# Kernel optimization log

Measured on AMD Instinct MI355X. Metric: run time of the kernel, lower is better.

## Reference

```python
import jax, jax.numpy as jnp
import numpy as np

N = 50000
E = 1280000
D = 64          # in_features = hidden_size = out_features
HEADS = 1
NEG_SLOPE = 0.2
EPS_COS = 1e-8
EPS_SM = 1e-16


def _xavier(key, shape):
    fan_in, fan_out = shape[0], shape[-1]
    lim = float(np.sqrt(6.0 / (fan_in + fan_out)))
    return jax.random.uniform(key, shape, jnp.float32, -lim, lim)


def setup_inputs() -> dict:
    key = jax.random.key(0)
    ks = jax.random.split(key, 16)
    x = jax.random.normal(ks[0], (N, D), jnp.float32)
    edge_index = jax.random.randint(ks[1], (2, E), 0, N, jnp.int64)
    edge_attr = jax.random.uniform(ks[2], (E,), jnp.float32)
    return {
        "x": x,
        "edge_index": edge_index,
        "edge_attr": edge_attr,
        # COSGAT layer 0 (in D -> out D, heads=1)
        "W0": _xavier(ks[3], (D, HEADS * D)),
        "att0": _xavier(ks[4], (HEADS, 2 * D)),
        "beta0": jnp.zeros((HEADS,), jnp.float32),
        "b0": jnp.zeros((HEADS * D,), jnp.float32),
        # COSGAT layer 1
        "W1": _xavier(ks[5], (D, HEADS * D)),
        "att1": _xavier(ks[6], (HEADS, 2 * D)),
        "beta1": jnp.zeros((HEADS,), jnp.float32),
        "b1": jnp.zeros((HEADS * D,), jnp.float32),
        # LinearEncoder residual branch
        "rW1": _xavier(ks[7], (D, D)),
        "rb1": jnp.zeros((D,), jnp.float32),
        "rW2": _xavier(ks[8], (D, D)),
        "rb2": jnp.zeros((D,), jnp.float32),
    }


def _seg_softmax(logits, idx, n):
    # softmax over edges grouped by target node idx; logits [E, H]
    m = jax.ops.segment_max(logits, idx, num_segments=n)
    ex = jnp.exp(logits - m[idx])
    s = jax.ops.segment_sum(ex, idx, num_segments=n)
    return ex / (s[idx] + EPS_SM)


def _cosgat(x, src, dst, w, W, att, beta, bias):
    n = x.shape[0]
    H = (x @ W).reshape(n, HEADS, -1)           # [N, H, C]
    Hi, Hj = H[dst], H[src]                      # [E, H, C]
    # GAT logits: att . [Hi || Hj]
    logits = (jnp.einsum('ehc,hc->eh', Hi, att[:, :H.shape[-1]])
              + jnp.einsum('ehc,hc->eh', Hj, att[:, H.shape[-1]:]))
    logits = jnp.where(logits >= 0, logits, NEG_SLOPE * logits)
    # cosine similarity on original features
    xi, xj = x[dst], x[src]
    ni = jnp.maximum(jnp.linalg.norm(xi, axis=-1), EPS_COS)
    nj = jnp.maximum(jnp.linalg.norm(xj, axis=-1), EPS_COS)
    cos = jnp.sum(xi * xj, axis=-1) / (ni * nj)  # [E]
    cos = jnp.broadcast_to(cos[:, None], logits.shape)
    gat_alpha = _seg_softmax(logits, dst, n)
    cos_alpha = _seg_softmax(cos, dst, n)
    b = jax.nn.sigmoid(beta)[None, :]            # [1, H]
    fused = (1.0 - b) * gat_alpha + b * cos_alpha
    w_cl = jnp.minimum(w, 4.0)
    gate = jnp.clip(1.0 - w_cl / 4.0, 0.0, 1.0)[:, None]  # [E, 1]
    final = _seg_softmax(fused * gate, dst, n)   # [E, H]
    msg = Hj * final[:, :, None]                 # [E, H, C]
    out = jax.ops.segment_sum(msg, dst, num_segments=n)
    out = out.reshape(n, -1) + bias              # concat heads + bias
    return jax.nn.elu(out)


def reference(x, edge_index, edge_attr, W0, att0, beta0, b0,
              W1, att1, beta1, b1, rW1, rb1, rW2, rb2):
    src, dst = edge_index[0], edge_index[1]      # PyG: i = target = edge_index[1]
    # residual MLP: Linear -> relu -> Linear (dropout p=0, eval)
    x_res = jax.nn.relu(x @ rW1 + rb1) @ rW2 + rb2
    h = _cosgat(x, src, dst, edge_attr, W0, att0, beta0, b0)
    h = jax.nn.elu(h)                            # inter-layer elu in encoder
    h = _cosgat(h, src, dst, edge_attr, W1, att1, beta1, b1)
    return h + x_res
```

## Files before the change

kernel.cpp:

```cpp
#include <hip/hip_runtime.h>
#include <hip/hip_bf16.h>
#include <math.h>


constexpr int D = 64;
constexpr int CAP = 64;
constexpr float NEG_SLOPE = 0.2f;
constexpr float EPS_COS = 1e-8f;
constexpr float EPS_SM = 1e-16f;

#if defined(__has_builtin)
#if __has_builtin(__builtin_amdgcn_cvt_pk_f32_fp8) && __has_builtin(__builtin_amdgcn_cvt_pk_fp8_f32)
#define HW_FP8 1
#endif
#endif

typedef float floatx2 __attribute__((ext_vector_type(2)));

__device__ __forceinline__ float wred_sum(float v) {
#pragma unroll
  for (int off = 32; off > 0; off >>= 1) v += __shfl_xor(v, off, 64);
  return v;
}
__device__ __forceinline__ float wred_max(float v) {
#pragma unroll
  for (int off = 32; off > 0; off >>= 1) v = fmaxf(v, __shfl_xor(v, off, 64));
  return v;
}
__device__ __forceinline__ float elu1(float x) { return x > 0.f ? x : __expf(x) - 1.f; }
__device__ __forceinline__ float sane(float v) {
  return (v == v && fabsf(v) < 1e30f) ? v : 0.f;
}
__device__ __forceinline__ float ldv(const void* p, size_t i, int f32) {
  return f32 ? ((const float*)p)[i]
             : __bfloat162float(((const __hip_bfloat16*)p)[i]);
}
__device__ __forceinline__ void stv(void* p, size_t i, int f32, float v) {
  if (f32) ((float*)p)[i] = v;
  else ((__hip_bfloat16*)p)[i] = __float2bfloat16(v);
}
__device__ __forceinline__ float b2f(unsigned short u) {
  return __uint_as_float(((unsigned int)u) << 16);
}
__device__ __forceinline__ void unp8(uint4 u, float* f) {
  f[0] = __uint_as_float(u.x << 16);
  f[1] = __uint_as_float(u.x & 0xffff0000u);
  f[2] = __uint_as_float(u.y << 16);
  f[3] = __uint_as_float(u.y & 0xffff0000u);
  f[4] = __uint_as_float(u.z << 16);
  f[5] = __uint_as_float(u.z & 0xffff0000u);
  f[6] = __uint_as_float(u.w << 16);
  f[7] = __uint_as_float(u.w & 0xffff0000u);
}

__device__ __forceinline__ unsigned char enc_fp8(float v) {
#ifdef HW_FP8
  int pk = __builtin_amdgcn_cvt_pk_fp8_f32(v, v, 0, false);
  return (unsigned char)(pk & 0xFF);
#else
  _Float16 h = (_Float16)v;
  unsigned short ub;
  __builtin_memcpy(&ub, &h, 2);
  return (unsigned char)((ub + 0x80) >> 8);
#endif
}
__device__ __forceinline__ void dec_fp8x8(uint2 u, float* f) {
#ifdef HW_FP8
  floatx2 a = __builtin_amdgcn_cvt_pk_f32_fp8(u.x, false);
  floatx2 b = __builtin_amdgcn_cvt_pk_f32_fp8(u.x, true);
  floatx2 c = __builtin_amdgcn_cvt_pk_f32_fp8(u.y, false);
  floatx2 d = __builtin_amdgcn_cvt_pk_f32_fp8(u.y, true);
  f[0] = a[0]; f[1] = a[1]; f[2] = b[0]; f[3] = b[1];
  f[4] = c[0]; f[5] = c[1]; f[6] = d[0]; f[7] = d[1];
#else
#pragma unroll
  for (int i = 0; i < 8; ++i) {
    unsigned int byte = (i < 4 ? (u.x >> (8 * i)) : (u.y >> (8 * (i - 4)))) & 0xFF;
    unsigned short hb = (unsigned short)(byte << 8);
    _Float16 h;
    __builtin_memcpy(&h, &hb, 2);
    f[i] = (float)h;
  }
#endif
}

__device__ __forceinline__ unsigned int pack_sg(int src, float g) {
  int gq = (int)(g * 16383.f + 0.5f);
  return ((unsigned int)src & 0x3FFFFu) | ((unsigned int)gq << 18);
}
__device__ __forceinline__ int upk_src(unsigned int e, int N) {
  return min((int)(e & 0x3FFFFu), N - 1);
}
__device__ __forceinline__ float upk_gate(unsigned int e) {
  return (float)(e >> 18) * (1.f / 16383.f);
}
__device__ __forceinline__ float gate_of(float w) {
  return fminf(fmaxf(1.f - 0.25f * fminf(w, 4.f), 0.f), 1.f);
}

__device__ float slow_cos(const unsigned char* __restrict__ fhat, int a, int b) {
  const uint2* fa = (const uint2*)(fhat + (size_t)a * D);
  const uint2* fb = (const uint2*)(fhat + (size_t)b * D);
  float dsum = 0.f;
  for (int q = 0; q < 8; ++q) {
    float va[8], vb[8];
    dec_fp8x8(fa[q], va);
    dec_fp8x8(fb[q], vb);
#pragma unroll
    for (int i = 0; i < 8; ++i) dsum += va[i] * vb[i];
  }
  return dsum;
}

__device__ __forceinline__ void prep_node(float f, int f32, int wid, int lane,
                                          const void* __restrict__ W,
                                          const void* __restrict__ att,
                                          unsigned char* __restrict__ fhat,
                                          __hip_bfloat16* __restrict__ Hmat,
                                          float* __restrict__ a_l,
                                          float* __restrict__ a_r,
                                          float* __restrict__ ls) {
  float n2 = wred_sum(f * f);
  float nrm = fmaxf(sqrtf(n2), EPS_COS);
  fhat[(size_t)wid * D + lane] = enc_fp8(f / nrm);
  ls[lane] = f;
  __syncthreads();
  float h0 = 0.f, h1 = 0.f, h2 = 0.f, h3 = 0.f;
  if (f32) {
    const float* Wf = (const float*)W;
#pragma unroll 4
    for (int k = 0; k < D; k += 4) {
      h0 += ls[k] * Wf[k * D + lane];
      h1 += ls[k + 1] * Wf[(k + 1) * D + lane];
      h2 += ls[k + 2] * Wf[(k + 2) * D + lane];
      h3 += ls[k + 3] * Wf[(k + 3) * D + lane];
    }
  } else {
    const __hip_bfloat16* Wb = (const __hip_bfloat16*)W;
#pragma unroll 4
    for (int k = 0; k < D; k += 4) {
      h0 += ls[k] * __bfloat162float(Wb[k * D + lane]);
      h1 += ls[k + 1] * __bfloat162float(Wb[(k + 1) * D + lane]);
      h2 += ls[k + 2] * __bfloat162float(Wb[(k + 2) * D + lane]);
      h3 += ls[k + 3] * __bfloat162float(Wb[(k + 3) * D + lane]);
    }
  }
  float Hc = (h0 + h1) + (h2 + h3);
  Hmat[(size_t)wid * D + lane] = __float2bfloat16(Hc);
  float al = wred_sum(Hc * ldv(att, lane, f32));
  float ar = wred_sum(Hc * ldv(att, D + lane, f32));
  if (lane == 0) {
    a_l[wid] = al;
    a_r[wid] = ar;
  }
  __syncthreads();
}

__global__ void __launch_bounds__(256) k_bin(const unsigned short* __restrict__ xu,
                                             const int* __restrict__ ei,
                                             const void* __restrict__ w,
                                             int* __restrict__ flags,
                                             int* __restrict__ cnt,
                                             unsigned int* __restrict__ csr2,
                                             int N, int E) {
  __shared__ int sf[2];
  const int tid = threadIdx.x;
  if (tid < 64) {
    float v = b2f(xu[tid]);
    float a = fabsf(v);
    unsigned long long m = __ballot(a > 1e-4f && a < 100.f);
    unsigned long long m2 = __ballot(ei[2 * tid + 1] != 0);
    if (tid == 0) {
      sf[0] = (__popcll(m) >= 60) ? 0 : 1;
      sf[1] = (m2 == 0ull) ? 1 : 0;
      if (blockIdx.x == 0) {
        flags[0] = sf[0];
        flags[1] = sf[1];
      }
    }
  }
  __syncthreads();
  const int f32 = sf[0], wide = sf[1];
  const int e0 = (blockIdx.x * 256 + tid) * 2;
  if (e0 >= E) return;
  const bool has1 = (e0 + 1 < E);
  int s0, s1, d0, d1;
  if (wide) {
    int4 vs = *(const int4*)(ei + 2 * (size_t)e0);
    int4 vd = *(const int4*)(ei + 2 * (size_t)E + 2 * (size_t)e0);
    s0 = vs.x; s1 = vs.z; d0 = vd.x; d1 = vd.z;
  } else {
    int2 vs = *(const int2*)(ei + e0);
    int2 vd = *(const int2*)(ei + (size_t)E + e0);
    s0 = vs.x; s1 = vs.y; d0 = vd.x; d1 = vd.y;
  }
  float w0, w1 = 0.f;
  if (f32) {
    float2 wv = *(const float2*)((const float*)w + e0);
    w0 = wv.x; w1 = wv.y;
  } else {
    const __hip_bfloat16* wb = (const __hip_bfloat16*)w;
    w0 = __bfloat162float(wb[e0]);
    if (has1) w1 = __bfloat162float(wb[e0 + 1]);
  }
  int d0c = min(max(d0, 0), N - 1);
  int slot0 = atomicAdd(&cnt[d0c], 1);
  if (slot0 < CAP)
    csr2[(size_t)d0c * CAP + slot0] = pack_sg(min(max(s0, 0), N - 1), gate_of(w0));
  if (has1) {
    int d1c = min(max(d1, 0), N - 1);
    int slot1 = atomicAdd(&cnt[d1c], 1);
    if (slot1 < CAP)
      csr2[(size_t)d1c * CAP + slot1] = pack_sg(min(max(s1, 0), N - 1), gate_of(w1));
  }
}

__global__ void __launch_bounds__(64, 4) k_prepW(const void* __restrict__ xin,
                                                 const void* __restrict__ W,
                                                 const void* __restrict__ att,
                                                 const int* __restrict__ flags,
                                                 unsigned char* __restrict__ fhat,
                                                 __hip_bfloat16* __restrict__ Hmat,
                                                 float* __restrict__ a_l,
                                                 float* __restrict__ a_r, int N) {
  __shared__ float ls[D];
  const int lane = threadIdx.x;
  const int f32 = flags[0];
  float wreg[D];
  if (f32) {
    const float* Wf = (const float*)W;
#pragma unroll
    for (int k = 0; k < D; ++k) wreg[k] = Wf[k * D + lane];
  } else {
    const __hip_bfloat16* Wb = (const __hip_bfloat16*)W;
#pragma unroll
    for (int k = 0; k < D; ++k) wreg[k] = __bfloat162float(Wb[k * D + lane]);
  }
  const float attl = ldv(att, lane, f32);
  const float attr = ldv(att, D + lane, f32);
  float f = (blockIdx.x < (unsigned)N) ? ldv(xin, (size_t)blockIdx.x * D + lane, f32) : 0.f;
  for (int wid = blockIdx.x; wid < N; wid += gridDim.x) {
    const int nwid = wid + gridDim.x;
    float fnx = (nwid < N) ? ldv(xin, (size_t)nwid * D + lane, f32) : 0.f;
    float n2 = wred_sum(f * f);
    float nrm = fmaxf(sqrtf(n2), EPS_COS);
    fhat[(size_t)wid * D + lane] = enc_fp8(f / nrm);
    ls[lane] = f;
    __syncthreads();
    float h0 = 0.f, h1 = 0.f, h2 = 0.f, h3 = 0.f;
#pragma unroll
    for (int k = 0; k < D; k += 4) {
      h0 += ls[k] * wreg[k];
      h1 += ls[k + 1] * wreg[k + 1];
      h2 += ls[k + 2] * wreg[k + 2];
      h3 += ls[k + 3] * wreg[k + 3];
    }
    float Hc = (h0 + h1) + (h2 + h3);
    Hmat[(size_t)wid * D + lane] = __float2bfloat16(Hc);
    float al = wred_sum(Hc * attl);
    float ar = wred_sum(Hc * attr);
    if (lane == 0) {
      a_l[wid] = al;
      a_r[wid] = ar;
    }
    __syncthreads();
    f = fnx;
  }
}

__global__ void __launch_bounds__(64, 3) k_resW(const void* __restrict__ xin,
                                                const void* __restrict__ rW1,
                                                const void* __restrict__ rb1,
                                                const void* __restrict__ rW2,
                                                const void* __restrict__ rb2,
                                                const int* __restrict__ flags,
                                                float* __restrict__ xres, int N) {
  __shared__ float ls[D];
  const int lane = threadIdx.x;
  const int f32 = flags[0];
  float w1reg[D], w2reg[D];
  if (f32) {
    const float* w1 = (const float*)rW1;
    const float* w2 = (const float*)rW2;
#pragma unroll
    for (int k = 0; k < D; ++k) w1reg[k] = w1[k * D + lane];
#pragma unroll
    for (int k = 0; k < D; ++k) w2reg[k] = w2[k * D + lane];
  } else {
    const __hip_bfloat16* w1 = (const __hip_bfloat16*)rW1;
    const __hip_bfloat16* w2 = (const __hip_bfloat16*)rW2;
#pragma unroll
    for (int k = 0; k < D; ++k) w1reg[k] = __bfloat162float(w1[k * D + lane]);
#pragma unroll
    for (int k = 0; k < D; ++k) w2reg[k] = __bfloat162float(w2[k * D + lane]);
  }
  const float b1v = ldv(rb1, lane, f32);
  const float b2v = ldv(rb2, lane, f32);
  float f = (blockIdx.x < (unsigned)N) ? ldv(xin, (size_t)blockIdx.x * D + lane, f32) : 0.f;
  for (int wid = blockIdx.x; wid < N; wid += gridDim.x) {
    const int nwid = wid + gridDim.x;
    float fnx = (nwid < N) ? ldv(xin, (size_t)nwid * D + lane, f32) : 0.f;
    ls[lane] = f;
    __syncthreads();
    float h0 = b1v, h1 = 0.f, h2 = 0.f, h3 = 0.f;
#pragma unroll
    for (int k = 0; k < D; k += 4) {
      h0 += ls[k] * w1reg[k];
      h1 += ls[k + 1] * w1reg[k + 1];
      h2 += ls[k + 2] * w1reg[k + 2];
      h3 += ls[k + 3] * w1reg[k + 3];
    }
    float tr = fmaxf((h0 + h1) + (h2 + h3), 0.f);
    __syncthreads();
    ls[lane] = tr;
    __syncthreads();
    float g0 = b2v, g1 = 0.f, g2 = 0.f, g3 = 0.f;
#pragma unroll
    for (int k = 0; k < D; k += 4) {
      g0 += ls[k] * w2reg[k];
      g1 += ls[k + 1] * w2reg[k + 1];
      g2 += ls[k + 2] * w2reg[k + 2];
      g3 += ls[k + 3] * w2reg[k + 3];
    }
    xres[(size_t)wid * D + lane] = (g0 + g1) + (g2 + g3);
    __syncthreads();
    f = fnx;
  }
}

__global__ void __launch_bounds__(64) k_prep(const void* __restrict__ xin,
                                             const void* __restrict__ W,
                                             const void* __restrict__ att,
                                             const int* __restrict__ flags,
                                             unsigned char* __restrict__ fhat,
                                             __hip_bfloat16* __restrict__ Hmat,
                                             float* __restrict__ a_l,
                                             float* __restrict__ a_r, int N) {
  __shared__ float ls[D];
  const int lane = threadIdx.x;
  const int wid = blockIdx.x;
  if (wid >= N) return;
  const int f32 = flags[0];
  float f = ldv(xin, (size_t)wid * D + lane, f32);
  prep_node(f, f32, wid, lane, W, att, fhat, Hmat, a_l, a_r, ls);
}

__global__ void __launch_bounds__(64, 8) k_edge(const int* __restrict__ cnt,
                                                const unsigned int* __restrict__ csr2,
                                                const int* __restrict__ ei,
                                                const void* __restrict__ w,
                                                const unsigned char* __restrict__ fhat,
                                                const __hip_bfloat16* __restrict__ Hmat,
                                                const float* __restrict__ a_l,
                                                const float* __restrict__ a_r,
                                                const void* __restrict__ beta,
                                                const void* __restrict__ bias,
                                                const void* __restrict__ x,
                                                const void* __restrict__ rW1,
                                                const void* __restrict__ rb1,
                                                const void* __restrict__ rW2,
                                                const void* __restrict__ rb2,
                                                const void* __restrict__ Wn,
                                                const void* __restrict__ attn,
                                                unsigned char* __restrict__ fh2,
                                                __hip_bfloat16* __restrict__ Hm2,
                                                float* __restrict__ al2,
                                                float* __restrict__ ar2,
                                                const float* __restrict__ xres,
                                                const int* __restrict__ flags,
                                                void* __restrict__ out,
                                                int N, int E, int mode) {
  const int lane = threadIdx.x;
  const int wid = blockIdx.x;
  __shared__ float2 lc[CAP];
  __shared__ float2 sg[CAP];
  __shared__ float lds_t[D];
  if (wid >= N) return;
  const int f32 = flags[0];
  const int g = lane >> 3;
  const int sub = lane & 7;
  const int degRaw = cnt[wid];
  const float aln = a_l[wid];
  const float bb = 1.f / (1.f + __expf(-ldv(beta, 0, f32)));
  const float ob = 1.f - bb;
  const char* HmatB = (const char*)Hmat;

  float v;
  if (degRaw <= CAP) {
    const int deg = degRaw;
    const int s = wid * CAP;
    float fn[8];
    dec_fp8x8(*(const uint2*)(fhat + (((unsigned)wid << 6) | ((unsigned)sub << 3))), fn);

    float m1 = -1e30f, m2 = -1e30f;
    uint4 hm[4];
#pragma unroll
    for (int kk = 0; kk < 4; ++kk) {
      const int base = kk * 8;
      if (base < deg) {
        const int j = base + g;
        const bool val = j < deg;
        const unsigned int en = val ? csr2[s + j] : (unsigned int)wid;
        const unsigned src = (unsigned)upk_src(en, N);
        float hv[8];
        dec_fp8x8(*(const uint2*)(fhat + ((src << 6) | ((unsigned)sub << 3))), hv);
        hm[kk] = *(const uint4*)(HmatB + ((src << 7) | ((unsigned)sub << 4)));
        float d = 0.f;
#pragma unroll
        for (int i = 0; i < 8; ++i) d += fn[i] * hv[i];
        d += __shfl_xor(d, 1, 64);
        d += __shfl_xor(d, 2, 64);
        d += __shfl_xor(d, 4, 64);
        float l = aln + a_r[src];
        l = (l >= 0.f) ? l : NEG_SLOPE * l;
        if (val) {
          m1 = fmaxf(m1, l);
          m2 = fmaxf(m2, d);
          if (sub == 0) lc[j] = make_float2(l, d);
        }
      }
    }
    for (int base = 32; base < deg; base += 8) {
      const int j = base + g;
      const bool val = j < deg;
      const unsigned int en = val ? csr2[s + j] : (unsigned int)wid;
      const unsigned src = (unsigned)upk_src(en, N);
      float hv[8];
      dec_fp8x8(*(const uint2*)(fhat + ((src << 6) | ((unsigned)sub << 3))), hv);
      float d = 0.f;
#pragma unroll
      for (int i = 0; i < 8; ++i) d += fn[i] * hv[i];
      d += __shfl_xor(d, 1, 64);
      d += __shfl_xor(d, 2, 64);
      d += __shfl_xor(d, 4, 64);
      float l = aln + a_r[src];
      l = (l >= 0.f) ? l : NEG_SLOPE * l;
      if (val) {
        m1 = fmaxf(m1, l);
        m2 = fmaxf(m2, d);
        if (sub == 0) lc[j] = make_float2(l, d);
      }
    }
    m1 = fmaxf(m1, __shfl_xor(m1, 8, 64));
    m1 = fmaxf(m1, __shfl_xor(m1, 16, 64));
    m1 = fmaxf(m1, __shfl_xor(m1, 32, 64));
    m2 = fmaxf(m2, __shfl_xor(m2, 8, 64));
    m2 = fmaxf(m2, __shfl_xor(m2, 16, 64));
    m2 = fmaxf(m2, __shfl_xor(m2, 32, 64));

    float el0 = 0.f, ec0 = 0.f, gg0 = 0.f;
    int q0 = 0;
    float ps1 = 0.f, ps2 = 0.f;
    if (lane < deg) {
      const unsigned int en = csr2[s + lane];
      q0 = upk_src(en, N);
      gg0 = upk_gate(en);
      float2 t = lc[lane];
      el0 = __expf(t.x - m1);
      ec0 = __expf(t.y - m2);
      ps1 = el0;
      ps2 = ec0;
    }
    const float rs1 = 1.f / (wred_sum(ps1) + EPS_SM);
    const float rs2 = 1.f / (wred_sum(ps2) + EPS_SM);

    float sp = 0.f;
    if (lane < deg) {
      float tt = (ob * el0 * rs1 + bb * ec0 * rs2) * gg0;
      float p0 = __expf(tt - 1.f);
      sp = p0;
      sg[lane] = make_float2(__int_as_float(q0), p0);
    }
    const float rinv = 1.f / (wred_sum(sp) + EPS_SM);

    float acc[8] = {0.f, 0.f, 0.f, 0.f, 0.f, 0.f, 0.f, 0.f};
#pragma unroll
    for (int kk = 0; kk < 4; ++kk) {
      const int base = kk * 8;
      if (base < deg) {
        const int j = base + g;
        const float pv = (j < deg) ? sg[j].y : 0.f;
        float hv[8];
        unp8(hm[kk], hv);
#pragma unroll
        for (int i = 0; i < 8; ++i) acc[i] += pv * hv[i];
      }
    }
    for (int base = 32; base < deg; base += 8) {
      const int j = base + g;
      float2 en = (j < deg) ? sg[j] : make_float2(__int_as_float(wid), 0.f);
      const float pv = en.y;
      const unsigned srcv = (unsigned)__float_as_int(en.x);
      float hv[8];
      unp8(*(const uint4*)(HmatB + ((srcv << 7) | ((unsigned)sub << 4))), hv);
#pragma unroll
      for (int i = 0; i < 8; ++i) acc[i] += pv * hv[i];
    }
#pragma unroll
    for (int i = 0; i < 8; ++i) {
      acc[i] += __shfl_xor(acc[i], 8, 64);
      acc[i] += __shfl_xor(acc[i], 16, 64);
      acc[i] += __shfl_xor(acc[i], 32, 64);
    }
    if (g == 0) {
#pragma unroll
      for (int i = 0; i < 8; ++i) lds_t[8 * sub + i] = acc[i];
    }
    v = lds_t[lane] * rinv + ldv(bias, lane, f32);
  } else {
    const int wide = flags[1];
    lds_t[lane] = 0.f;
    float m1 = -1e30f, m2 = -1e30f;
    for (int e64 = lane; e64 < E; e64 += 64) {
      int dd = wide ? ei[2 * (size_t)E + 2 * (size_t)e64] : ei[(size_t)E + e64];
      if (dd != wid) continue;
      int ss = wide ? ei[2 * (size_t)e64] : ei[e64];
      ss = min(max(ss, 0), N - 1);
      float l = aln + a_r[ss];
      l = (l >= 0.f) ? l : NEG_SLOPE * l;
      float c = slow_cos(fhat, wid, ss);
      m1 = fmaxf(m1, l);
      m2 = fmaxf(m2, c);
    }
    m1 = wred_max(m1);
    m2 = wred_max(m2);
    float ps1 = 0.f, ps2 = 0.f;
    for (int e64 = lane; e64 < E; e64 += 64) {
      int dd = wide ? ei[2 * (size_t)E + 2 * (size_t)e64] : ei[(size_t)E + e64];
      if (dd != wid) continue;
      int ss = wide ? ei[2 * (size_t)e64] : ei[e64];
      ss = min(max(ss, 0), N - 1);
      float l = aln + a_r[ss];
      l = (l >= 0.f) ? l : NEG_SLOPE * l;
      float c = slow_cos(fhat, wid, ss);
      ps1 += __expf(l - m1);
      ps2 += __expf(c - m2);
    }
    const float rs1 = 1.f / (wred_sum(ps1) + EPS_SM);
    const float rs2 = 1.f / (wred_sum(ps2) + EPS_SM);
    float sp = 0.f;
    for (int e64 = lane; e64 < E; e64 += 64) {
      int dd = wide ? ei[2 * (size_t)E + 2 * (size_t)e64] : ei[(size_t)E + e64];
      if (dd != wid) continue;
      int ss = wide ? ei[2 * (size_t)e64] : ei[e64];
      ss = min(max(ss, 0), N - 1);
      float l = aln + a_r[ss];
      l = (l >= 0.f) ? l : NEG_SLOPE * l;
      float c = slow_cos(fhat, wid, ss);
      float gx = gate_of(ldv(w, e64, f32));
      float px = __expf((ob * __expf(l - m1) * rs1 + bb * __expf(c - m2) * rs2) * gx - 1.f);
      sp += px;
      for (int q = 0; q < D; ++q)
        atomicAdd(&lds_t[q], px * __bfloat162float(Hmat[(size_t)ss * D + q]));
    }
    const float rinv = 1.f / (wred_sum(sp) + EPS_SM);
    v = lds_t[lane] * rinv + ldv(bias, lane, f32);
  }

  v = elu1(v);
  if (mode == 3) {
    float a2 = xres[(size_t)wid * D + lane];
    stv(out, (size_t)wid * D + lane, f32, sane(v + a2));
  } else if (mode == 1) {
    float xv = ldv(x, (size_t)wid * D + lane, f32);
    float b0_ = ldv(rb1, lane, f32);
    __syncthreads();
    lds_t[lane] = xv;
    __syncthreads();
    float a2;
    float h0 = 0.f, h1 = 0.f, h2 = 0.f, h3 = 0.f;
    if (f32) {
      const float* w1 = (const float*)rW1;
      const float* w2 = (const float*)rW2;
#pragma unroll 4
      for (int k = 0; k < D; k += 4) {
        h0 += lds_t[k] * w1[k * D + lane];
        h1 += lds_t[k + 1] * w1[(k + 1) * D + lane];
        h2 += lds_t[k + 2] * w1[(k + 2) * D + lane];
        h3 += lds_t[k + 3] * w1[(k + 3) * D + lane];
      }
      float tr = fmaxf(b0_ + (h0 + h1) + (h2 + h3), 0.f);
      __syncthreads();
      lds_t[lane] = tr;
      __syncthreads();
      float g0 = 0.f, g1 = 0.f, g2 = 0.f, g3 = 0.f;
#pragma unroll 4
      for (int k = 0; k < D; k += 4) {
        g0 += lds_t[k] * w2[k * D + lane];
        g1 += lds_t[k + 1] * w2[(k + 1) * D + lane];
        g2 += lds_t[k + 2] * w2[(k + 2) * D + lane];
        g3 += lds_t[k + 3] * w2[(k + 3) * D + lane];
      }
      a2 = ((const float*)rb2)[lane] + (g0 + g1) + (g2 + g3);
    } else {
      const __hip_bfloat16* w1 = (const __hip_bfloat16*)rW1;
      const __hip_bfloat16* w2 = (const __hip_bfloat16*)rW2;
#pragma unroll 4
      for (int k = 0; k < D; k += 4) {
        h0 += lds_t[k] * __bfloat162float(w1[k * D + lane]);
        h1 += lds_t[k + 1] * __bfloat162float(w1[(k + 1) * D + lane]);
        h2 += lds_t[k + 2] * __bfloat162float(w1[(k + 2) * D + lane]);
        h3 += lds_t[k + 3] * __bfloat162float(w1[(k + 3) * D + lane]);
      }
      float tr = fmaxf(b0_ + (h0 + h1) + (h2 + h3), 0.f);
      __syncthreads();
      lds_t[lane] = tr;
      __syncthreads();
      float g0 = 0.f, g1 = 0.f, g2 = 0.f, g3 = 0.f;
#pragma unroll 4
      for (int k = 0; k < D; k += 4) {
        g0 += lds_t[k] * __bfloat162float(w2[k * D + lane]);
        g1 += lds_t[k + 1] * __bfloat162float(w2[(k + 1) * D + lane]);
        g2 += lds_t[k + 2] * __bfloat162float(w2[(k + 2) * D + lane]);
        g3 += lds_t[k + 3] * __bfloat162float(w2[(k + 3) * D + lane]);
      }
      a2 = __bfloat162float(((const __hip_bfloat16*)rb2)[lane]) + (g0 + g1) + (g2 + g3);
    }
    stv(out, (size_t)wid * D + lane, f32, sane(v + a2));
  } else {
    v = elu1(v);
    if (mode == 0) {
      __syncthreads();
      prep_node(sane(v), f32, wid, lane, Wn, attn, fh2, Hm2, al2, ar2, lds_t);
    } else {
      stv(out, (size_t)wid * D + lane, f32, sane(v));
    }
  }
}

extern "C" void kernel_launch(void* const* d_in, const int* in_sizes, int n_in,
                              void* d_out, int out_size, void* d_ws, size_t ws_size,
                              hipStream_t stream) {
  const void* x = d_in[0];
  const int* ei = (const int*)d_in[1];
  const void* w = d_in[2];
  const void* W0 = d_in[3];
  const void* att0 = d_in[4];
  const void* beta0 = d_in[5];
  const void* b0 = d_in[6];
  const void* W1 = d_in[7];
  const void* att1 = d_in[8];
  const void* beta1 = d_in[9];
  const void* b1 = d_in[10];
  const void* rW1 = d_in[11];
  const void* rb1 = d_in[12];
  const void* rW2 = d_in[13];
  const void* rb2 = d_in[14];

  const int N = in_sizes[0] / D;
  const int E = in_sizes[2];

  char* base = (char*)d_ws;
  size_t off = 0;
  auto alloc = [&](size_t bytes) -> void* {
    void* p = base + off;
    off += (bytes + 255) & ~(size_t)255;
    return p;
  };
  int* flags = (int*)alloc(256);
  int* cnt = (int*)alloc((size_t)N * 4);
  unsigned int* csr2 = (unsigned int*)alloc((size_t)N * CAP * 4);
  unsigned char* fhat = (unsigned char*)alloc((size_t)N * D);
  __hip_bfloat16* Hmat = (__hip_bfloat16*)alloc((size_t)N * D * 2);
  float* a_l = (float*)alloc((size_t)N * 4);
  float* a_r = (float*)alloc((size_t)N * 4);
  const size_t common_off = off;
  float* hbuf = (float*)alloc((size_t)N * D * 4);
  float* xres = (float*)alloc((size_t)N * D * 4);
  const bool tierA = (off <= ws_size);
  off = common_off;
  unsigned char* fhat2 = (unsigned char*)alloc((size_t)N * D);
  __hip_bfloat16* Hmat2 = (__hip_bfloat16*)alloc((size_t)N * D * 2);
  float* a_l2 = (float*)alloc((size_t)N * 4);
  float* a_r2 = (float*)alloc((size_t)N * 4);
  const bool tierB = (off <= ws_size);

  const int eb2 = (E / 2 + 255) / 256;

  hipMemsetAsync(cnt, 0, (size_t)N * 4, stream);
  k_bin<<<eb2, 256, 0, stream>>>((const unsigned short*)x, ei, w, flags, cnt,
                                 csr2, N, E);

  if (tierA) {
    k_prepW<<<4096, 64, 0, stream>>>(x, W0, att0, flags, fhat, Hmat, a_l, a_r, N);
    k_resW<<<3072, 64, 0, stream>>>(x, rW1, rb1, rW2, rb2, flags, xres, N);
    k_edge<<<N, 64, 0, stream>>>(cnt, csr2, ei, w, fhat, Hmat, a_l, a_r,
                                 beta0, b0, x, rW1, rb1, rW2, rb2,
                                 nullptr, nullptr, nullptr, nullptr, nullptr, nullptr,
                                 nullptr, flags, hbuf, N, E, 2);
    k_prepW<<<4096, 64, 0, stream>>>(hbuf, W1, att1, flags, fhat, Hmat, a_l, a_r, N);
    k_edge<<<N, 64, 0, stream>>>(cnt, csr2, ei, w, fhat, Hmat, a_l, a_r,
                                 beta1, b1, x, rW1, rb1, rW2, rb2,
                                 nullptr, nullptr, nullptr, nullptr, nullptr, nullptr,
                                 xres, flags, d_out, N, E, 3);
  } else if (tierB) {
    k_prep<<<N, 64, 0, stream>>>(x, W0, att0, flags, fhat, Hmat, a_l, a_r, N);
    k_edge<<<N, 64, 0, stream>>>(cnt, csr2, ei, w, fhat, Hmat, a_l, a_r,
                                 beta0, b0, x, rW1, rb1, rW2, rb2,
                                 W1, att1, fhat2, Hmat2, a_l2, a_r2,
                                 nullptr, flags, d_out, N, E, 0);
    k_edge<<<N, 64, 0, stream>>>(cnt, csr2, ei, w, fhat2, Hmat2, a_l2, a_r2,
                                 beta1, b1, x, rW1, rb1, rW2, rb2,
                                 nullptr, nullptr, nullptr, nullptr, nullptr, nullptr,
                                 nullptr, flags, d_out, N, E, 1);
  } else {
    k_prep<<<N, 64, 0, stream>>>(x, W0, att0, flags, fhat, Hmat, a_l, a_r, N);
    k_edge<<<N, 64, 0, stream>>>(cnt, csr2, ei, w, fhat, Hmat, a_l, a_r,
                                 beta0, b0, x, rW1, rb1, rW2, rb2,
                                 nullptr, nullptr, nullptr, nullptr, nullptr, nullptr,
                                 nullptr, flags, d_out, N, E, 2);
    k_prep<<<N, 64, 0, stream>>>(d_out, W1, att1, flags, fhat, Hmat, a_l, a_r, N);
    k_edge<<<N, 64, 0, stream>>>(cnt, csr2, ei, w, fhat, Hmat, a_l, a_r,
                                 beta1, b1, x, rW1, rb1, rW2, rb2,
                                 nullptr, nullptr, nullptr, nullptr, nullptr, nullptr,
                                 nullptr, flags, d_out, N, E, 1);
  }
}
```

Measured before the change: 366.3 us.

## Fuse edge binning, layer-0 prep and residual MLP into one kernel with bucketed scatter

Replaces the separate k_bin, k_prepW and k_resW launches with a single per-node kernel. Each block bins a slice of edges and then does node prep plus the residual MLP. Edges are first appended to coarse destination buckets and a follow-up k_bucket kernel scatters them into per-node CSR slots. This is meant to localize the atomics and CSR writes and to cut launch count. The cost is an extra bucket buffer and kernel, and the residual weights are now read from global memory per node instead of being held in registers across a persistent loop.

New measurement: 604.2 us. 1.65x slower.

```diff
diff --git a/kernel.cpp b/kernel.cpp
--- a/kernel.cpp
+++ b/kernel.cpp
@@ -5,6 +5,7 @@
 
 constexpr int D = 64;
 constexpr int CAP = 64;
+constexpr int NBK = 1024;
 constexpr float NEG_SLOPE = 0.2f;
 constexpr float EPS_COS = 1e-8f;
 constexpr float EPS_SM = 1e-16f;
@@ -154,6 +155,135 @@
     a_r[wid] = ar;
   }
   __syncthreads();
+}
+
+__global__ void __launch_bounds__(64) k_all(const unsigned short* __restrict__ xu,
+                                            const int* __restrict__ ei,
+                                            const void* __restrict__ w,
+                                            int* __restrict__ flags,
+                                            int* __restrict__ cnt,
+                                            int* __restrict__ bcnt,
+                                            uint2* __restrict__ bkt, int bcap,
+                                            const void* __restrict__ x,
+                                            const void* __restrict__ W,
+                                            const void* __restrict__ att,
+                                            const void* __restrict__ rW1,
+                                            const void* __restrict__ rb1,
+                                            const void* __restrict__ rW2,
+                                            const void* __restrict__ rb2,
+                                            unsigned char* __restrict__ fhat,
+                                            __hip_bfloat16* __restrict__ Hmat,
+                                            float* __restrict__ a_l,
+                                            float* __restrict__ a_r,
+                                            float* __restrict__ xres,
+                                            unsigned int* __restrict__ csr2,
+                                            int N, int E) {
+  __shared__ float ls[D];
+  const int lane = threadIdx.x;
+  const int b = blockIdx.x;
+  float dv = b2f(xu[lane]);
+  float da = fabsf(dv);
+  unsigned long long m = __ballot(da > 1e-4f && da < 100.f);
+  unsigned long long m2 = __ballot(ei[2 * lane + 1] != 0);
+  const int f32 = (__popcll(m) >= 60) ? 0 : 1;
+  const int wide = (m2 == 0ull) ? 1 : 0;
+  if (b == 0 && lane == 0) {
+    flags[0] = f32;
+    flags[1] = wide;
+  }
+  const long long e0 = ((long long)b * E) / N;
+  const long long e1 = ((long long)(b + 1) * E) / N;
+  for (long long e = e0 + lane; e < e1; e += 64) {
+    int ss, dd;
+    if (wide) {
+      ss = ei[2 * e];
+      dd = ei[2 * (size_t)E + 2 * e];
+    } else {
+      ss = ei[e];
+      dd = ei[(size_t)E + e];
+    }
+    float we = ldv(w, (size_t)e, f32);
+    const int dc = min(max(dd, 0), N - 1);
+    const unsigned int sg = pack_sg(min(max(ss, 0), N - 1), gate_of(we));
+    bool direct = true;
+    if (bcap > 0) {
+      const int bu = (int)(((long long)dc * NBK) / N);
+      const int pos = atomicAdd(&bcnt[bu], 1);
+      if (pos < bcap) {
+        bkt[(size_t)bu * bcap + pos] = make_uint2(sg, (unsigned)dc);
+        direct = false;
+      }
+    }
+    if (direct) {
+      const int slot = atomicAdd(&cnt[dc], 1);
+      if (slot < CAP) csr2[(size_t)dc * CAP + slot] = sg;
+    }
+  }
+  if (b >= N) return;
+  float f = ldv(x, (size_t)b * D + lane, f32);
+  prep_node(f, f32, b, lane, W, att, fhat, Hmat, a_l, a_r, ls);
+  ls[lane] = f;
+  __syncthreads();
+  float h0 = ldv(rb1, lane, f32), h1 = 0.f, h2 = 0.f, h3 = 0.f;
+  if (f32) {
+    const float* w1 = (const float*)rW1;
+#pragma unroll 4
+    for (int k = 0; k < D; k += 4) {
+      h0 += ls[k] * w1[k * D + lane];
+      h1 += ls[k + 1] * w1[(k + 1) * D + lane];
+      h2 += ls[k + 2] * w1[(k + 2) * D + lane];
+      h3 += ls[k + 3] * w1[(k + 3) * D + lane];
+    }
+  } else {
+    const __hip_bfloat16* w1 = (const __hip_bfloat16*)rW1;
+#pragma unroll 4
+    for (int k = 0; k < D; k += 4) {
+      h0 += ls[k] * __bfloat162float(w1[k * D + lane]);
+      h1 += ls[k + 1] * __bfloat162float(w1[(k + 1) * D + lane]);
+      h2 += ls[k + 2] * __bfloat162float(w1[(k + 2) * D + lane]);
+      h3 += ls[k + 3] * __bfloat162float(w1[(k + 3) * D + lane]);
+    }
+  }
+  float tr = fmaxf((h0 + h1) + (h2 + h3), 0.f);
+  __syncthreads();
+  ls[lane] = tr;
+  __syncthreads();
+  float g0 = ldv(rb2, lane, f32), g1 = 0.f, g2 = 0.f, g3 = 0.f;
+  if (f32) {
+    const float* w2 = (const float*)rW2;
+#pragma unroll 4
+    for (int k = 0; k < D; k += 4) {
+      g0 += ls[k] * w2[k * D + lane];
+      g1 += ls[k + 1] * w2[(k + 1) * D + lane];
+      g2 += ls[k + 2] * w2[(k + 2) * D + lane];
+      g3 += ls[k + 3] * w2[(k + 3) * D + lane];
+    }
+  } else {
+    const __hip_bfloat16* w2 = (const __hip_bfloat16*)rW2;
+#pragma unroll 4
+    for (int k = 0; k < D; k += 4) {
+      g0 += ls[k] * __bfloat162float(w2[k * D + lane]);
+      g1 += ls[k + 1] * __bfloat162float(w2[(k + 1) * D + lane]);
+      g2 += ls[k + 2] * __bfloat162float(w2[(k + 2) * D + lane]);
+      g3 += ls[k + 3] * __bfloat162float(w2[(k + 3) * D + lane]);
+    }
+  }
+  xres[(size_t)b * D + lane] = (g0 + g1) + (g2 + g3);
+}
+
+__global__ void __launch_bounds__(256) k_bucket(const int* __restrict__ bcnt,
+                                                const uint2* __restrict__ bkt, int bcap,
+                                                int* __restrict__ cnt,
+                                                unsigned int* __restrict__ csr2, int N) {
+  const int bu = blockIdx.x;
+  const int n = min(bcnt[bu], bcap);
+  const uint2* base = bkt + (size_t)bu * bcap;
+  for (int i = threadIdx.x; i < n; i += 256) {
+    uint2 en = base[i];
+    const int dc = min((int)en.y, N - 1);
+    const int slot = atomicAdd(&cnt[dc], 1);
+    if (slot < CAP) csr2[(size_t)dc * CAP + slot] = en.x;
+  }
 }
 
 __global__ void __launch_bounds__(256) k_bin(const unsigned short* __restrict__ xu,
@@ -263,66 +393,6 @@
       a_l[wid] = al;
       a_r[wid] = ar;
     }
-    __syncthreads();
-    f = fnx;
-  }
-}
-
-__global__ void __launch_bounds__(64, 3) k_resW(const void* __restrict__ xin,
-                                                const void* __restrict__ rW1,
-                                                const void* __restrict__ rb1,
-                                                const void* __restrict__ rW2,
-                                                const void* __restrict__ rb2,
-                                                const int* __restrict__ flags,
-                                                float* __restrict__ xres, int N) {
-  __shared__ float ls[D];
-  const int lane = threadIdx.x;
-  const int f32 = flags[0];
-  float w1reg[D], w2reg[D];
-  if (f32) {
-    const float* w1 = (const float*)rW1;
-    const float* w2 = (const float*)rW2;
-#pragma unroll
-    for (int k = 0; k < D; ++k) w1reg[k] = w1[k * D + lane];
-#pragma unroll
-    for (int k = 0; k < D; ++k) w2reg[k] = w2[k * D + lane];
-  } else {
-    const __hip_bfloat16* w1 = (const __hip_bfloat16*)rW1;
-    const __hip_bfloat16* w2 = (const __hip_bfloat16*)rW2;
-#pragma unroll
-    for (int k = 0; k < D; ++k) w1reg[k] = __bfloat162float(w1[k * D + lane]);
-#pragma unroll
-    for (int k = 0; k < D; ++k) w2reg[k] = __bfloat162float(w2[k * D + lane]);
-  }
-  const float b1v = ldv(rb1, lane, f32);
-  const float b2v = ldv(rb2, lane, f32);
-  float f = (blockIdx.x < (unsigned)N) ? ldv(xin, (size_t)blockIdx.x * D + lane, f32) : 0.f;
-  for (int wid = blockIdx.x; wid < N; wid += gridDim.x) {
-    const int nwid = wid + gridDim.x;
-    float fnx = (nwid < N) ? ldv(xin, (size_t)nwid * D + lane, f32) : 0.f;
-    ls[lane] = f;
-    __syncthreads();
-    float h0 = b1v, h1 = 0.f, h2 = 0.f, h3 = 0.f;
-#pragma unroll
-    for (int k = 0; k < D; k += 4) {
-      h0 += ls[k] * w1reg[k];
-      h1 += ls[k + 1] * w1reg[k + 1];
-      h2 += ls[k + 2] * w1reg[k + 2];
-      h3 += ls[k + 3] * w1reg[k + 3];
-    }
-    float tr = fmaxf((h0 + h1) + (h2 + h3), 0.f);
-    __syncthreads();
-    ls[lane] = tr;
-    __syncthreads();
-    float g0 = b2v, g1 = 0.f, g2 = 0.f, g3 = 0.f;
-#pragma unroll
-    for (int k = 0; k < D; k += 4) {
-      g0 += ls[k] * w2reg[k];
-      g1 += ls[k + 1] * w2reg[k + 1];
-      g2 += ls[k + 2] * w2reg[k + 2];
-      g3 += ls[k + 3] * w2reg[k + 3];
-    }
-    xres[(size_t)wid * D + lane] = (g0 + g1) + (g2 + g3);
     __syncthreads();
     f = fnx;
   }
@@ -668,6 +738,10 @@
   float* hbuf = (float*)alloc((size_t)N * D * 4);
   float* xres = (float*)alloc((size_t)N * D * 4);
   const bool tierA = (off <= ws_size);
+  const int bcap = 2 * (E / NBK) + 64;
+  int* bcnt = (int*)alloc((size_t)NBK * 4);
+  uint2* bkt = (uint2*)alloc((size_t)NBK * (size_t)bcap * 8);
+  const bool tierBk = (off <= ws_size);
   off = common_off;
   unsigned char* fhat2 = (unsigned char*)alloc((size_t)N * D);
   __hip_bfloat16* Hmat2 = (__hip_bfloat16*)alloc((size_t)N * D * 2);
@@ -678,12 +752,15 @@
   const int eb2 = (E / 2 + 255) / 256;
 
   hipMemsetAsync(cnt, 0, (size_t)N * 4, stream);
-  k_bin<<<eb2, 256, 0, stream>>>((const unsigned short*)x, ei, w, flags, cnt,
-                                 csr2, N, E);
 
   if (tierA) {
-    k_prepW<<<4096, 64, 0, stream>>>(x, W0, att0, flags, fhat, Hmat, a_l, a_r, N);
-    k_resW<<<3072, 64, 0, stream>>>(x, rW1, rb1, rW2, rb2, flags, xres, N);
+    const int usedBcap = tierBk ? bcap : 0;
+    if (tierBk) hipMemsetAsync(bcnt, 0, (size_t)NBK * 4, stream);
+    k_all<<<N, 64, 0, stream>>>((const unsigned short*)x, ei, w, flags, cnt,
+                                bcnt, bkt, usedBcap, x, W0, att0,
+                                rW1, rb1, rW2, rb2,
+                                fhat, Hmat, a_l, a_r, xres, csr2, N, E);
+    if (tierBk) k_bucket<<<NBK, 256, 0, stream>>>(bcnt, bkt, bcap, cnt, csr2, N);
     k_edge<<<N, 64, 0, stream>>>(cnt, csr2, ei, w, fhat, Hmat, a_l, a_r,
                                  beta0, b0, x, rW1, rb1, rW2, rb2,
                                  nullptr, nullptr, nullptr, nullptr, nullptr, nullptr,
@@ -694,6 +771,8 @@
                                  nullptr, nullptr, nullptr, nullptr, nullptr, nullptr,
                                  xres, flags, d_out, N, E, 3);
   } else if (tierB) {
+    k_bin<<<eb2, 256, 0, stream>>>((const unsigned short*)x, ei, w, flags, cnt,
+                                   csr2, N, E);
     k_prep<<<N, 64, 0, stream>>>(x, W0, att0, flags, fhat, Hmat, a_l, a_r, N);
     k_edge<<<N, 64, 0, stream>>>(cnt, csr2, ei, w, fhat, Hmat, a_l, a_r,
                                  beta0, b0, x, rW1, rb1, rW2, rb2,
@@ -704,6 +783,8 @@
                                  nullptr, nullptr, nullptr, nullptr, nullptr, nullptr,
                                  nullptr, flags, d_out, N, E, 1);
   } else {
+    k_bin<<<eb2, 256, 0, stream>>>((const unsigned short*)x, ei, w, flags, cnt,
+                                   csr2, N, E);
     k_prep<<<N, 64, 0, stream>>>(x, W0, att0, flags, fhat, Hmat, a_l, a_r, N);
     k_edge<<<N, 64, 0, stream>>>(cnt, csr2, ei, w, fhat, Hmat, a_l, a_r,
                                  beta0, b0, x, rW1, rb1, rW2, rb2,
```

## Replace direct CSR binning with two-pass partitioned scatter by destination range

Applied to the files above, without the earlier changes.

The single-pass k_bin, which atomically appends each edge into a per-destination CSR slot straight from global memory, is replaced by a two-stage scheme. k_scat bins edges in LDS into 64 destination-range partitions and writes them contiguously to a partition buffer. k_part then performs the per-node atomic insertion one partition per block, so the scattered writes stay in a narrow address window. This aims to improve locality of the random atomics and stores, at the cost of an extra pass over the edges and an extra workspace buffer. Overflow edges fall back to direct insertion, and the old path is kept for smaller workspaces.

Result: faster. 358.0 us (-2.3%).

```diff
diff --git a/kernel.cpp b/kernel.cpp
--- a/kernel.cpp
+++ b/kernel.cpp
@@ -5,6 +5,8 @@
 
 constexpr int D = 64;
 constexpr int CAP = 64;
+constexpr int NPART = 64;
+constexpr int EPB_MAX = 2048;
 constexpr float NEG_SLOPE = 0.2f;
 constexpr float EPS_COS = 1e-8f;
 constexpr float EPS_SM = 1e-16f;
@@ -154,6 +156,107 @@
     a_r[wid] = ar;
   }
   __syncthreads();
+}
+
+__global__ void __launch_bounds__(256) k_scat(const unsigned short* __restrict__ xu,
+                                              const int* __restrict__ ei,
+                                              const void* __restrict__ w,
+                                              int* __restrict__ flags,
+                                              int* __restrict__ cnt,
+                                              int* __restrict__ pcnt,
+                                              uint2* __restrict__ part, int pcap,
+                                              unsigned int* __restrict__ csr2,
+                                              int N, int E, int GB) {
+  __shared__ uint2 buf[EPB_MAX];
+  __shared__ uint2 srt[EPB_MAX];
+  __shared__ int hist[NPART], hoff[NPART], hcur[NPART], gbase[NPART];
+  __shared__ int sf[2];
+  const int tid = threadIdx.x;
+  if (tid < 64) {
+    float v = b2f(xu[tid]);
+    float a = fabsf(v);
+    unsigned long long m = __ballot(a > 1e-4f && a < 100.f);
+    unsigned long long m2 = __ballot(ei[2 * tid + 1] != 0);
+    if (tid == 0) {
+      sf[0] = (__popcll(m) >= 60) ? 0 : 1;
+      sf[1] = (m2 == 0ull) ? 1 : 0;
+      if (blockIdx.x == 0) {
+        flags[0] = sf[0];
+        flags[1] = sf[1];
+      }
+    }
+  }
+  __syncthreads();
+  const int f32 = sf[0], wide = sf[1];
+  const long long E0 = ((long long)blockIdx.x * E) / GB;
+  const long long E1 = ((long long)(blockIdx.x + 1) * E) / GB;
+  for (long long c0 = E0; c0 < E1; c0 += EPB_MAX) {
+    const int n = (int)min((long long)EPB_MAX, E1 - c0);
+    for (int i = tid; i < NPART; i += 256) hist[i] = 0;
+    __syncthreads();
+    for (int i = tid; i < n; i += 256) {
+      const long long e = c0 + i;
+      int ss, dd;
+      if (wide) {
+        ss = ei[2 * e];
+        dd = ei[2 * (size_t)E + 2 * e];
+      } else {
+        ss = ei[e];
+        dd = ei[(size_t)E + e];
+      }
+      float we = ldv(w, (size_t)e, f32);
+      const int dc = min(max(dd, 0), N - 1);
+      const unsigned sg = pack_sg(min(max(ss, 0), N - 1), gate_of(we));
+      buf[i] = make_uint2(sg, (unsigned)dc);
+      atomicAdd(&hist[(int)(((long long)dc * NPART) / N)], 1);
+    }
+    __syncthreads();
+    if (tid == 0) {
+      int acc = 0;
+      for (int p = 0; p < NPART; ++p) {
+        hoff[p] = acc;
+        hcur[p] = acc;
+        acc += hist[p];
+      }
+    }
+    __syncthreads();
+    if (tid < NPART) gbase[tid] = atomicAdd(&pcnt[tid], hist[tid]);
+    __syncthreads();
+    for (int i = tid; i < n; i += 256) {
+      uint2 en = buf[i];
+      const int p = (int)(((long long)en.y * NPART) / N);
+      const int pos = atomicAdd(&hcur[p], 1);
+      srt[pos] = en;
+    }
+    __syncthreads();
+    for (int i = tid; i < n; i += 256) {
+      uint2 en = srt[i];
+      const int p = (int)(((long long)en.y * NPART) / N);
+      const int idx = gbase[p] + (i - hoff[p]);
+      if (idx < pcap) {
+        part[(size_t)p * pcap + idx] = en;
+      } else {
+        const int slot = atomicAdd(&cnt[en.y], 1);
+        if (slot < CAP) csr2[(size_t)en.y * CAP + slot] = en.x;
+      }
+    }
+    __syncthreads();
+  }
+}
+
+__global__ void __launch_bounds__(1024) k_part(const int* __restrict__ pcnt,
+                                               const uint2* __restrict__ part, int pcap,
+                                               int* __restrict__ cnt,
+                                               unsigned int* __restrict__ csr2, int N) {
+  const int p = blockIdx.x;
+  const int np = min(pcnt[p], pcap);
+  const uint2* base = part + (size_t)p * pcap;
+  for (int i = threadIdx.x; i < np; i += 1024) {
+    uint2 en = base[i];
+    const int dc = min((int)en.y, N - 1);
+    const int slot = atomicAdd(&cnt[dc], 1);
+    if (slot < CAP) csr2[(size_t)dc * CAP + slot] = en.x;
+  }
 }
 
 __global__ void __launch_bounds__(256) k_bin(const unsigned short* __restrict__ xu,
@@ -667,6 +770,13 @@
   const size_t common_off = off;
   float* hbuf = (float*)alloc((size_t)N * D * 4);
   float* xres = (float*)alloc((size_t)N * D * 4);
+  int* pcnt = (int*)alloc((size_t)NPART * 4);
+  const int pcap = E / NPART + E / (NPART * 8) + 512;
+  uint2* part = (uint2*)alloc((size_t)NPART * (size_t)pcap * 8);
+  const bool tierR = (off <= ws_size);
+  off = common_off;
+  float* hbufA = (float*)alloc((size_t)N * D * 4);
+  float* xresA = (float*)alloc((size_t)N * D * 4);
   const bool tierA = (off <= ws_size);
   off = common_off;
   unsigned char* fhat2 = (unsigned char*)alloc((size_t)N * D);
@@ -676,12 +786,15 @@
   const bool tierB = (off <= ws_size);
 
   const int eb2 = (E / 2 + 255) / 256;
+  const int GB = 1024;
 
   hipMemsetAsync(cnt, 0, (size_t)N * 4, stream);
-  k_bin<<<eb2, 256, 0, stream>>>((const unsigned short*)x, ei, w, flags, cnt,
-                                 csr2, N, E);
-
-  if (tierA) {
+
+  if (tierR) {
+    hipMemsetAsync(pcnt, 0, (size_t)NPART * 4, stream);
+    k_scat<<<GB, 256, 0, stream>>>((const unsigned short*)x, ei, w, flags, cnt,
+                                   pcnt, part, pcap, csr2, N, E, GB);
+    k_part<<<NPART, 1024, 0, stream>>>(pcnt, part, pcap, cnt, csr2, N);
     k_prepW<<<4096, 64, 0, stream>>>(x, W0, att0, flags, fhat, Hmat, a_l, a_r, N);
     k_resW<<<3072, 64, 0, stream>>>(x, rW1, rb1, rW2, rb2, flags, xres, N);
     k_edge<<<N, 64, 0, stream>>>(cnt, csr2, ei, w, fhat, Hmat, a_l, a_r,
@@ -693,7 +806,23 @@
                                  beta1, b1, x, rW1, rb1, rW2, rb2,
                                  nullptr, nullptr, nullptr, nullptr, nullptr, nullptr,
                                  xres, flags, d_out, N, E, 3);
+  } else if (tierA) {
+    k_bin<<<eb2, 256, 0, stream>>>((const unsigned short*)x, ei, w, flags, cnt,
+                                   csr2, N, E);
+    k_prepW<<<4096, 64, 0, stream>>>(x, W0, att0, flags, fhat, Hmat, a_l, a_r, N);
+    k_resW<<<3072, 64, 0, stream>>>(x, rW1, rb1, rW2, rb2, flags, xresA, N);
+    k_edge<<<N, 64, 0, stream>>>(cnt, csr2, ei, w, fhat, Hmat, a_l, a_r,
+                                 beta0, b0, x, rW1, rb1, rW2, rb2,
+                                 nullptr, nullptr, nullptr, nullptr, nullptr, nullptr,
+                                 nullptr, flags, hbufA, N, E, 2);
+    k_prepW<<<4096, 64, 0, stream>>>(hbufA, W1, att1, flags, fhat, Hmat, a_l, a_r, N);
+    k_edge<<<N, 64, 0, stream>>>(cnt, csr2, ei, w, fhat, Hmat, a_l, a_r,
+                                 beta1, b1, x, rW1, rb1, rW2, rb2,
+                                 nullptr, nullptr, nullptr, nullptr, nullptr, nullptr,
+                                 xresA, flags, d_out, N, E, 3);
   } else if (tierB) {
+    k_bin<<<eb2, 256, 0, stream>>>((const unsigned short*)x, ei, w, flags, cnt,
+                                   csr2, N, E);
     k_prep<<<N, 64, 0, stream>>>(x, W0, att0, flags, fhat, Hmat, a_l, a_r, N);
     k_edge<<<N, 64, 0, stream>>>(cnt, csr2, ei, w, fhat, Hmat, a_l, a_r,
                                  beta0, b0, x, rW1, rb1, rW2, rb2,
@@ -704,6 +833,8 @@
                                  nullptr, nullptr, nullptr, nullptr, nullptr, nullptr,
                                  nullptr, flags, d_out, N, E, 1);
   } else {
+    k_bin<<<eb2, 256, 0, stream>>>((const unsigned short*)x, ei, w, flags, cnt,
+                                   csr2, N, E);
     k_prep<<<N, 64, 0, stream>>>(x, W0, att0, flags, fhat, Hmat, a_l, a_r, N);
     k_edge<<<N, 64, 0, stream>>>(cnt, csr2, ei, w, fhat, Hmat, a_l, a_r,
                                  beta0, b0, x, rW1, rb1, rW2, rb2,
```
